# Performance work log

Measured on AMD Instinct MI355X. Metric: run time of the kernel, lower is better.

Reference implementation:

```python
import jax, jax.numpy as jnp
import numpy as np

B, S, D_IN, D_OUT, H = 2, 2048, 1024, 1024, 16
HD = D_OUT // H

def setup_inputs() -> dict:
    key = jax.random.key(0)
    ks = jax.random.split(key, 6)
    sc_in = 1.0 / np.sqrt(D_IN)
    sc_out = 1.0 / np.sqrt(D_OUT)
    return {
        "x": jax.random.normal(ks[0], (B, S, D_IN), dtype=jnp.float32),
        "Wq": jax.random.uniform(ks[1], (D_IN, D_OUT), jnp.float32, -sc_in, sc_in),
        "Wk": jax.random.uniform(ks[2], (D_IN, D_OUT), jnp.float32, -sc_in, sc_in),
        "Wv": jax.random.uniform(ks[3], (D_IN, D_OUT), jnp.float32, -sc_in, sc_in),
        "Wo": jax.random.uniform(ks[4], (D_OUT, D_OUT), jnp.float32, -sc_out, sc_out),
        "bo": jax.random.uniform(ks[5], (D_OUT,), jnp.float32, -sc_out, sc_out),
    }

def reference(x, Wq, Wk, Wv, Wo, bo):
    b, s, _ = x.shape
    # QKV projections (no bias), split heads -> [b, h, s, hd]
    q = (x @ Wq).reshape(b, s, H, HD).transpose(0, 2, 1, 3)
    k = (x @ Wk).reshape(b, s, H, HD).transpose(0, 2, 1, 3)
    v = (x @ Wv).reshape(b, s, H, HD).transpose(0, 2, 1, 3)
    scores = jnp.einsum('bhqd,bhkd->bhqk', q, k)
    causal = jnp.triu(jnp.ones((s, s), dtype=bool), k=1)
    scores = jnp.where(causal, -jnp.inf, scores)
    w = jax.nn.softmax(scores / np.sqrt(HD), axis=-1)  # dropout p=0.0 -> identity
    ctx = jnp.einsum('bhqk,bhkd->bhqd', w, v)
    ctx = ctx.transpose(0, 2, 1, 3).reshape(b, s, D_OUT)
    return ctx @ Wo + bo
```

## Files before the change

### kernel.cpp

```cpp
#include <hip/hip_runtime.h>
#include <stdint.h>

typedef unsigned short u16;
typedef __attribute__((ext_vector_type(8))) short short8;
typedef __attribute__((ext_vector_type(4))) float floatx4;
typedef __attribute__((ext_vector_type(4))) u16 ushort4v;

typedef __attribute__((address_space(1))) const uint32_t gu32;
typedef __attribute__((address_space(3))) uint32_t lu32;

#define MFMA(a, b, c) __builtin_amdgcn_mfma_f32_16x16x32_bf16((a), (b), (c), 0, 0, 0)

__device__ __forceinline__ u16 f2bf(float f) {
    union { float f; uint32_t u; } x; x.f = f;
    uint32_t u = x.u;
    u += 0x7fffu + ((u >> 16) & 1u);
    return (u16)(u >> 16);
}

__device__ __forceinline__ uint32_t cvtpk_bf16(float lo, float hi) {
    uint32_t r;
    asm("v_cvt_pk_bf16_f32 %0, %1, %2" : "=v"(r) : "v"(lo), "v"(hi));
    return r;
}

__device__ __forceinline__ float fexp2(float x) {
#if defined(__has_builtin)
#if __has_builtin(__builtin_amdgcn_exp2f)
    return __builtin_amdgcn_exp2f(x);
#else
    return exp2f(x);
#endif
#else
    return exp2f(x);
#endif
}

__device__ __forceinline__ void async16(u16* lds, const u16* g) {
    __builtin_amdgcn_global_load_lds((gu32*)g, (lu32*)lds, 16, 0, 0);
}

#define KV8(buf, row, byteInRow) \
    (*(short8*)((char*)(buf) + (((row) << 7) + ((byteInRow) ^ (((row) & 7) << 4)))))

#define Q_SCALE_LOG2E 0.18033688011112042f

__global__ __launch_bounds__(256) void prep_kernel(
    const float* __restrict__ x,
    const float* __restrict__ W0, const float* __restrict__ W1,
    const float* __restrict__ W2, const float* __restrict__ W3,
    u16* __restrict__ WT, u16* __restrict__ Xbf)
{
    const int z = blockIdx.z;
    const int tx = threadIdx.x, ty = threadIdx.y;
    if (z == 4) {
        const int bid = blockIdx.y * 32 + blockIdx.x;
        const int t = ty * 32 + tx;
        const size_t base = ((size_t)bid * 256 + t) * 16;
        const float* xf = x + base;
        short8 v0, v1;
#pragma unroll
        for (int j = 0; j < 8; j++) v0[j] = (short)f2bf(xf[j]);
#pragma unroll
        for (int j = 0; j < 8; j++) v1[j] = (short)f2bf(xf[8 + j]);
        *(short8*)&Xbf[base] = v0;
        *(short8*)&Xbf[base + 8] = v1;
        return;
    }
    __shared__ u16 tile[32][33];
    const float* W = (z == 0) ? W0 : (z == 1) ? W1 : (z == 2) ? W2 : W3;
    u16* dst = WT + (size_t)z * 1024 * 1024;
    const int n0 = blockIdx.x * 32, k0 = blockIdx.y * 32;
#pragma unroll
    for (int i = 0; i < 4; i++)
        tile[ty + i * 8][tx] = f2bf(W[(size_t)(k0 + ty + i * 8) * 1024 + n0 + tx]);
    __syncthreads();
#pragma unroll
    for (int i = 0; i < 4; i++)
        dst[(size_t)(n0 + ty + i * 8) * 1024 + k0 + tx] = tile[tx][ty + i * 8];
}

__global__ __launch_bounds__(256) void gemm_qkv_kernel(
    const u16* __restrict__ X, const u16* __restrict__ WT,
    u16* __restrict__ Q, u16* __restrict__ Kout, u16* __restrict__ VT)
{
    __shared__ __align__(16) u16 As[128 * 32];
    __shared__ __align__(16) u16 Bs[128 * 32];
    const int bid = blockIdx.x;
    const int xcd = bid & 7;
    const int idx = bid >> 3;
    const int mat = idx >> 5;
    const int rr  = (idx >> 3) & 3;
    const int nn  = idx & 7;
    const int m0 = (xcd * 4 + rr) * 128;
    const int n0 = nn * 128;
    const u16* BW = WT + (size_t)mat * 1024 * 1024;
    const int tid = threadIdx.x;
    const int wave = tid >> 6, lane = tid & 63;
    const int lrow = lane & 15, lquad = lane >> 4;
    const int wr = (wave >> 1) * 64, wc = (wave & 1) * 64;

    const int ci0 = wave * 128 + lane;
    const int ci1 = ci0 + 64;
    const int ar0 = ci0 >> 2, ac0 = (ci0 & 3) * 8;
    const int ar1 = ci1 >> 2, ac1 = (ci1 & 3) * 8;
    u16* ldsA0 = As + (size_t)(wave * 128) * 8;
    u16* ldsA1 = As + (size_t)(wave * 128 + 64) * 8;
    u16* ldsB0 = Bs + (size_t)(wave * 128) * 8;
    u16* ldsB1 = Bs + (size_t)(wave * 128 + 64) * 8;
    const u16* gA0 = &X[(size_t)(m0 + ar0) * 1024 + ac0];
    const u16* gA1 = &X[(size_t)(m0 + ar1) * 1024 + ac1];
    const u16* gB0 = &BW[(size_t)(n0 + ar0) * 1024 + ac0];
    const u16* gB1 = &BW[(size_t)(n0 + ar1) * 1024 + ac1];

    floatx4 acc[4][4];
#pragma unroll
    for (int mt = 0; mt < 4; mt++)
#pragma unroll
        for (int nt = 0; nt < 4; nt++) acc[mt][nt] = (floatx4){0.f, 0.f, 0.f, 0.f};

    for (int k0 = 0; k0 < 1024; k0 += 32) {
        __syncthreads();
        async16(ldsA0, gA0 + k0);
        async16(ldsA1, gA1 + k0);
        async16(ldsB0, gB0 + k0);
        async16(ldsB1, gB1 + k0);
        __syncthreads();
        short8 af[4], bf[4];
#pragma unroll
        for (int mt = 0; mt < 4; mt++)
            af[mt] = *(const short8*)&As[(wr + mt * 16 + lrow) * 32 + lquad * 8];
#pragma unroll
        for (int nt = 0; nt < 4; nt++)
            bf[nt] = *(const short8*)&Bs[(wc + nt * 16 + lrow) * 32 + lquad * 8];
#pragma unroll
        for (int mt = 0; mt < 4; mt++)
#pragma unroll
            for (int nt = 0; nt < 4; nt++)
                acc[mt][nt] = MFMA(af[mt], bf[nt], acc[mt][nt]);
    }

    const float qs = (mat == 0) ? Q_SCALE_LOG2E : 1.0f;
#pragma unroll
    for (int mt = 0; mt < 4; mt++) {
        const int gm = m0 + wr + mt * 16 + lquad * 4;
        const int b_ = gm >> 11;
        const int s  = gm & 2047;
#pragma unroll
        for (int nt = 0; nt < 4; nt++) {
            const int gn = n0 + wc + nt * 16 + lrow;
            const int h = gn >> 6, hd = gn & 63;
            const int bh = b_ * 16 + h;
            if (mat == 2) {
                ushort4v v;
#pragma unroll
                for (int i = 0; i < 4; i++) v[i] = f2bf(acc[mt][nt][i]);
                *(ushort4v*)&VT[((size_t)bh * 64 + hd) * 2048 + s] = v;
            } else {
                u16* dst = (mat == 0) ? Q : Kout;
#pragma unroll
                for (int i = 0; i < 4; i++)
                    dst[((size_t)bh * 2048 + s + i) * 64 + hd] = f2bf(acc[mt][nt][i] * qs);
            }
        }
    }
}

__global__ __launch_bounds__(256, 4) void attn_kernel(
    const u16* __restrict__ Q, const u16* __restrict__ Kk,
    const u16* __restrict__ VT, u16* __restrict__ ctx)
{
    __shared__ __align__(16) u16 Ks[64 * 64];
    __shared__ __align__(16) u16 Vs[64 * 64];
    __shared__ __align__(16) u16 P[4][16][80];
    const int tid = threadIdx.x, wave = tid >> 6, lane = tid & 63;
    const int lrow = lane & 15, lquad = lane >> 4;
    const float NEGINF = -__builtin_inff();

    const int bh = blockIdx.x & 31;
    const int g = blockIdx.x >> 5;
    const int qb = (g < 16) ? (31 - g) : (g - 16);
    const int ntiles = qb + 1;
    const int q0 = qb * 64 + wave * 16;

    const u16* Qb = Q  + (size_t)bh * 2048 * 64;
    const u16* Kb = Kk + (size_t)bh * 2048 * 64;
    const u16* Vb = VT + (size_t)bh * 64 * 2048;

    const short8 qf0 = *(const short8*)&Qb[(size_t)(q0 + lrow) * 64 + lquad * 8];
    const short8 qf1 = *(const short8*)&Qb[(size_t)(q0 + lrow) * 64 + 32 + lquad * 8];

    const int myq = q0 + lrow;
    float m_s = NEGINF, l_s = 0.f;
    floatx4 o[4];
#pragma unroll
    for (int i = 0; i < 4; i++) o[i] = (floatx4){0.f, 0.f, 0.f, 0.f};

    const int r0 = tid >> 3, r1 = r0 + 32;
    const int ce = (tid & 7) * 8;
    const int cb = (tid & 7) * 16;

    short8 kreg0 = *(const short8*)&Kb[(size_t)r0 * 64 + ce];
    short8 kreg1 = *(const short8*)&Kb[(size_t)r1 * 64 + ce];
    short8 vreg0 = *(const short8*)&Vb[(size_t)r0 * 2048 + ce];
    short8 vreg1 = *(const short8*)&Vb[(size_t)r1 * 2048 + ce];

    for (int kt = 0; kt < ntiles; kt++) {
        __syncthreads();
        KV8(Ks, r0, cb) = kreg0;
        KV8(Ks, r1, cb) = kreg1;
        KV8(Vs, r0, cb) = vreg0;
        KV8(Vs, r1, cb) = vreg1;
        if (kt + 1 < ntiles) {
            kreg0 = *(const short8*)&Kb[(size_t)((kt + 1) * 64 + r0) * 64 + ce];
            kreg1 = *(const short8*)&Kb[(size_t)((kt + 1) * 64 + r1) * 64 + ce];
            vreg0 = *(const short8*)&Vb[(size_t)r0 * 2048 + (kt + 1) * 64 + ce];
            vreg1 = *(const short8*)&Vb[(size_t)r1 * 2048 + (kt + 1) * 64 + ce];
        }
        __syncthreads();

        floatx4 s[4];
#pragma unroll
        for (int nt = 0; nt < 4; nt++) {
            const short8 kf0 = KV8(Ks, nt * 16 + lrow, lquad * 16);
            const short8 kf1 = KV8(Ks, nt * 16 + lrow, 64 + lquad * 16);
            floatx4 a = (floatx4){0.f, 0.f, 0.f, 0.f};
            a = MFMA(kf0, qf0, a);
            a = MFMA(kf1, qf1, a);
            s[nt] = a;
        }

        if (kt == ntiles - 1) {
#pragma unroll
            for (int nt = 0; nt < 4; nt++)
#pragma unroll
                for (int i = 0; i < 4; i++)
                    if (kt * 64 + nt * 16 + lquad * 4 + i > myq) s[nt][i] = NEGINF;
        }

        float mx = NEGINF;
#pragma unroll
        for (int nt = 0; nt < 4; nt++)
            mx = fmaxf(mx, fmaxf(fmaxf(s[nt][0], s[nt][1]),
                                 fmaxf(s[nt][2], s[nt][3])));
        mx = fmaxf(mx, __shfl_xor(mx, 16));
        mx = fmaxf(mx, __shfl_xor(mx, 32));

        if (!__all(mx <= m_s + 8.0f)) {
            const float mnew = fmaxf(m_s, mx);
            const float alpha = fexp2(m_s - mnew);
            m_s = mnew;
            l_s *= alpha;
#pragma unroll
            for (int ht = 0; ht < 4; ht++)
#pragma unroll
                for (int i = 0; i < 4; i++) o[ht][i] *= alpha;
        }

        float sum = 0.f;
#pragma unroll
        for (int nt = 0; nt < 4; nt++)
#pragma unroll
            for (int i = 0; i < 4; i++) {
                const float pv = fexp2(s[nt][i] - m_s);
                s[nt][i] = pv;
                sum += pv;
            }
        sum += __shfl_xor(sum, 16);
        sum += __shfl_xor(sum, 32);
        l_s += sum;

#pragma unroll
        for (int nt = 0; nt < 4; nt++) {
            uint2 pk;
            pk.x = cvtpk_bf16(s[nt][0], s[nt][1]);
            pk.y = cvtpk_bf16(s[nt][2], s[nt][3]);
            *(uint2*)&P[wave][lrow][nt * 16 + lquad * 4] = pk;
        }
#pragma unroll
        for (int st = 0; st < 2; st++) {
            const short8 pf = *(const short8*)&P[wave][lrow][st * 32 + lquad * 8];
#pragma unroll
            for (int ht = 0; ht < 4; ht++) {
                const short8 vf = KV8(Vs, ht * 16 + lrow, st * 64 + lquad * 16);
                o[ht] = MFMA(vf, pf, o[ht]);
            }
        }
    }

    const int b_ = bh >> 4, h_ = bh & 15;
    const float inv_l = 1.0f / l_s;
#pragma unroll
    for (int ht = 0; ht < 4; ht++) {
        uint2 pk;
        pk.x = cvtpk_bf16(o[ht][0] * inv_l, o[ht][1] * inv_l);
        pk.y = cvtpk_bf16(o[ht][2] * inv_l, o[ht][3] * inv_l);
        *(uint2*)&ctx[((size_t)(b_ * 2048 + q0 + lrow)) * 1024 + h_ * 64 + ht * 16 + lquad * 4] = pk;
    }
}

__global__ __launch_bounds__(256) void gemm_out_kernel(
    const u16* __restrict__ X, const u16* __restrict__ WT,
    const float* __restrict__ bias, float* __restrict__ out)
{
    __shared__ __align__(16) u16 As[128 * 32];
    __shared__ __align__(16) u16 Bs[128 * 32];
    const int bid = blockIdx.x;
    const int xcd = bid & 7;
    const int idx = bid >> 3;
    const int rr  = idx >> 3;
    const int nn  = idx & 7;
    const int m0 = (xcd * 4 + rr) * 128;
    const int n0 = nn * 128;
    const int tid = threadIdx.x;
    const int wave = tid >> 6, lane = tid & 63;
    const int lrow = lane & 15, lquad = lane >> 4;
    const int wr = (wave >> 1) * 64, wc = (wave & 1) * 64;

    const int ci0 = wave * 128 + lane;
    const int ci1 = ci0 + 64;
    const int ar0 = ci0 >> 2, ac0 = (ci0 & 3) * 8;
    const int ar1 = ci1 >> 2, ac1 = (ci1 & 3) * 8;
    u16* ldsA0 = As + (size_t)(wave * 128) * 8;
    u16* ldsA1 = As + (size_t)(wave * 128 + 64) * 8;
    u16* ldsB0 = Bs + (size_t)(wave * 128) * 8;
    u16* ldsB1 = Bs + (size_t)(wave * 128 + 64) * 8;
    const u16* gA0 = &X[(size_t)(m0 + ar0) * 1024 + ac0];
    const u16* gA1 = &X[(size_t)(m0 + ar1) * 1024 + ac1];
    const u16* gB0 = &WT[(size_t)(n0 + ar0) * 1024 + ac0];
    const u16* gB1 = &WT[(size_t)(n0 + ar1) * 1024 + ac1];

    floatx4 acc[4][4];
#pragma unroll
    for (int mt = 0; mt < 4; mt++)
#pragma unroll
        for (int nt = 0; nt < 4; nt++) acc[mt][nt] = (floatx4){0.f, 0.f, 0.f, 0.f};

    for (int k0 = 0; k0 < 1024; k0 += 32) {
        __syncthreads();
        async16(ldsA0, gA0 + k0);
        async16(ldsA1, gA1 + k0);
        async16(ldsB0, gB0 + k0);
        async16(ldsB1, gB1 + k0);
        __syncthreads();
        short8 af[4], bf[4];
#pragma unroll
        for (int mt = 0; mt < 4; mt++)
            af[mt] = *(const short8*)&As[(wr + mt * 16 + lrow) * 32 + lquad * 8];
#pragma unroll
        for (int nt = 0; nt < 4; nt++)
            bf[nt] = *(const short8*)&Bs[(wc + nt * 16 + lrow) * 32 + lquad * 8];
#pragma unroll
        for (int mt = 0; mt < 4; mt++)
#pragma unroll
            for (int nt = 0; nt < 4; nt++)
                acc[mt][nt] = MFMA(af[mt], bf[nt], acc[mt][nt]);
    }

#pragma unroll
    for (int mt = 0; mt < 4; mt++) {
        const int gm = m0 + wr + mt * 16 + lquad * 4;
#pragma unroll
        for (int nt = 0; nt < 4; nt++) {
            const int gn = n0 + wc + nt * 16 + lrow;
            const float bv = bias[gn];
#pragma unroll
            for (int i = 0; i < 4; i++)
                out[(size_t)(gm + i) * 1024 + gn] = acc[mt][nt][i] + bv;
        }
    }
}

extern "C" void kernel_launch(void* const* d_in, const int* in_sizes, int n_in,
                              void* d_out, int out_size, void* d_ws, size_t ws_size,
                              hipStream_t stream) {
    u16* ws = (u16*)d_ws + 64;

    const size_t MB1 = 1024 * 1024;
    u16* WT   = ws;
    u16* Qw   = ws + 4 * MB1;
    u16* Kw   = ws + 8 * MB1;
    u16* VTw  = ws + 12 * MB1;
    u16* ctxw = ws + 16 * MB1;
    u16* Xbf  = ws + 20 * MB1;

    prep_kernel<<<dim3(32, 32, 5), dim3(32, 8), 0, stream>>>(
        (const float*)d_in[0], (const float*)d_in[1], (const float*)d_in[2],
        (const float*)d_in[3], (const float*)d_in[4], WT, Xbf);
    gemm_qkv_kernel<<<768, 256, 0, stream>>>(Xbf, WT, Qw, Kw, VTw);
    attn_kernel<<<1024, 256, 0, stream>>>(Qw, Kw, VTw, ctxw);
    gemm_out_kernel<<<256, 256, 0, stream>>>(ctxw, WT + 3 * MB1, (const float*)d_in[5], (float*)d_out);
}
```

Measured before the change: 191.7 us.

## Double-buffer LDS tiles in QKV and output GEMMs to overlap loads with MFMA

Both projection GEMM kernels now use two LDS buffers per operand. The next K-slice is issued asynchronously into one buffer while MFMAs consume the other. This halves the barriers per K step and aims to hide global-load latency behind compute. It doubles LDS use per block, which may reduce occupancy, and relies on async copies completing before the following barrier.

```diff
diff --git a/kernel.cpp b/kernel.cpp
--- a/kernel.cpp
+++ b/kernel.cpp
@@ -80,12 +80,34 @@
         dst[(size_t)(n0 + ty + i * 8) * 1024 + k0 + tx] = tile[tx][ty + i * 8];
 }
 
+#define GSTAGE(AB, BB, kk) do { \
+    async16((AB) + (wave * 128) * 8,      gA0 + (kk)); \
+    async16((AB) + (wave * 128 + 64) * 8, gA1 + (kk)); \
+    async16((BB) + (wave * 128) * 8,      gB0 + (kk)); \
+    async16((BB) + (wave * 128 + 64) * 8, gB1 + (kk)); \
+} while (0)
+
+#define GCOMPUTE(AB, BB) do { \
+    short8 af[4], bfv[4]; \
+    _Pragma("unroll") \
+    for (int mt = 0; mt < 4; mt++) \
+        af[mt] = *(const short8*)&(AB)[(wr + mt * 16 + lrow) * 32 + lquad * 8]; \
+    _Pragma("unroll") \
+    for (int nt = 0; nt < 4; nt++) \
+        bfv[nt] = *(const short8*)&(BB)[(wc + nt * 16 + lrow) * 32 + lquad * 8]; \
+    _Pragma("unroll") \
+    for (int mt = 0; mt < 4; mt++) \
+        _Pragma("unroll") \
+        for (int nt = 0; nt < 4; nt++) \
+            acc[mt][nt] = MFMA(af[mt], bfv[nt], acc[mt][nt]); \
+} while (0)
+
 __global__ __launch_bounds__(256) void gemm_qkv_kernel(
     const u16* __restrict__ X, const u16* __restrict__ WT,
     u16* __restrict__ Q, u16* __restrict__ Kout, u16* __restrict__ VT)
 {
-    __shared__ __align__(16) u16 As[128 * 32];
-    __shared__ __align__(16) u16 Bs[128 * 32];
+    __shared__ __align__(16) u16 As0[128 * 32], As1[128 * 32];
+    __shared__ __align__(16) u16 Bs0[128 * 32], Bs1[128 * 32];
     const int bid = blockIdx.x;
     const int xcd = bid & 7;
     const int idx = bid >> 3;
@@ -104,10 +126,6 @@
     const int ci1 = ci0 + 64;
     const int ar0 = ci0 >> 2, ac0 = (ci0 & 3) * 8;
     const int ar1 = ci1 >> 2, ac1 = (ci1 & 3) * 8;
-    u16* ldsA0 = As + (size_t)(wave * 128) * 8;
-    u16* ldsA1 = As + (size_t)(wave * 128 + 64) * 8;
-    u16* ldsB0 = Bs + (size_t)(wave * 128) * 8;
-    u16* ldsB1 = Bs + (size_t)(wave * 128 + 64) * 8;
     const u16* gA0 = &X[(size_t)(m0 + ar0) * 1024 + ac0];
     const u16* gA1 = &X[(size_t)(m0 + ar1) * 1024 + ac1];
     const u16* gB0 = &BW[(size_t)(n0 + ar0) * 1024 + ac0];
@@ -119,25 +137,15 @@
 #pragma unroll
         for (int nt = 0; nt < 4; nt++) acc[mt][nt] = (floatx4){0.f, 0.f, 0.f, 0.f};
 
-    for (int k0 = 0; k0 < 1024; k0 += 32) {
-        __syncthreads();
-        async16(ldsA0, gA0 + k0);
-        async16(ldsA1, gA1 + k0);
-        async16(ldsB0, gB0 + k0);
-        async16(ldsB1, gB1 + k0);
-        __syncthreads();
-        short8 af[4], bf[4];
-#pragma unroll
-        for (int mt = 0; mt < 4; mt++)
-            af[mt] = *(const short8*)&As[(wr + mt * 16 + lrow) * 32 + lquad * 8];
-#pragma unroll
-        for (int nt = 0; nt < 4; nt++)
-            bf[nt] = *(const short8*)&Bs[(wc + nt * 16 + lrow) * 32 + lquad * 8];
-#pragma unroll
-        for (int mt = 0; mt < 4; mt++)
-#pragma unroll
-            for (int nt = 0; nt < 4; nt++)
-                acc[mt][nt] = MFMA(af[mt], bf[nt], acc[mt][nt]);
+    GSTAGE(As0, Bs0, 0);
+    __syncthreads();
+    for (int k0 = 0; k0 < 1024; k0 += 64) {
+        GSTAGE(As1, Bs1, k0 + 32);
+        GCOMPUTE(As0, Bs0);
+        __syncthreads();
+        if (k0 + 64 < 1024) GSTAGE(As0, Bs0, k0 + 64);
+        GCOMPUTE(As1, Bs1);
+        __syncthreads();
     }
 
     const float qs = (mat == 0) ? Q_SCALE_LOG2E : 1.0f;
@@ -303,8 +311,8 @@
     const u16* __restrict__ X, const u16* __restrict__ WT,
     const float* __restrict__ bias, float* __restrict__ out)
 {
-    __shared__ __align__(16) u16 As[128 * 32];
-    __shared__ __align__(16) u16 Bs[128 * 32];
+    __shared__ __align__(16) u16 As0[128 * 32], As1[128 * 32];
+    __shared__ __align__(16) u16 Bs0[128 * 32], Bs1[128 * 32];
     const int bid = blockIdx.x;
     const int xcd = bid & 7;
     const int idx = bid >> 3;
@@ -321,10 +329,6 @@
     const int ci1 = ci0 + 64;
     const int ar0 = ci0 >> 2, ac0 = (ci0 & 3) * 8;
     const int ar1 = ci1 >> 2, ac1 = (ci1 & 3) * 8;
-    u16* ldsA0 = As + (size_t)(wave * 128) * 8;
-    u16* ldsA1 = As + (size_t)(wave * 128 + 64) * 8;
-    u16* ldsB0 = Bs + (size_t)(wave * 128) * 8;
-    u16* ldsB1 = Bs + (size_t)(wave * 128 + 64) * 8;
     const u16* gA0 = &X[(size_t)(m0 + ar0) * 1024 + ac0];
     const u16* gA1 = &X[(size_t)(m0 + ar1) * 1024 + ac1];
     const u16* gB0 = &WT[(size_t)(n0 + ar0) * 1024 + ac0];
@@ -336,25 +340,15 @@
 #pragma unroll
         for (int nt = 0; nt < 4; nt++) acc[mt][nt] = (floatx4){0.f, 0.f, 0.f, 0.f};
 
-    for (int k0 = 0; k0 < 1024; k0 += 32) {
-        __syncthreads();
-        async16(ldsA0, gA0 + k0);
-        async16(ldsA1, gA1 + k0);
-        async16(ldsB0, gB0 + k0);
-        async16(ldsB1, gB1 + k0);
-        __syncthreads();
-        short8 af[4], bf[4];
-#pragma unroll
-        for (int mt = 0; mt < 4; mt++)
-            af[mt] = *(const short8*)&As[(wr + mt * 16 + lrow) * 32 + lquad * 8];
-#pragma unroll
-        for (int nt = 0; nt < 4; nt++)
-            bf[nt] = *(const short8*)&Bs[(wc + nt * 16 + lrow) * 32 + lquad * 8];
-#pragma unroll
-        for (int mt = 0; mt < 4; mt++)
-#pragma unroll
-            for (int nt = 0; nt < 4; nt++)
-                acc[mt][nt] = MFMA(af[mt], bf[nt], acc[mt][nt]);
+    GSTAGE(As0, Bs0, 0);
+    __syncthreads();
+    for (int k0 = 0; k0 < 1024; k0 += 64) {
+        GSTAGE(As1, Bs1, k0 + 32);
+        GCOMPUTE(As0, Bs0);
+        __syncthreads();
+        if (k0 + 64 < 1024) GSTAGE(As0, Bs0, k0 + 64);
+        GCOMPUTE(As1, Bs1);
+        __syncthreads();
     }
 
 #pragma unroll
```

Result: faster. 187.8 us (-2.0%).
